# Kernel tuning notes

Hardware: AMD Instinct MI355X
Metric: run time of the kernel (lower is better)

Reference implementation:

```python
import jax, jax.numpy as jnp
import numpy as np

N_NODES, NUM_GRAPHS, MAX_N = 65536, 512, 192
D, H = 512, 8
DH = D // H


def setup_inputs() -> dict:
    key = jax.random.key(0)
    ks = jax.random.split(key, 13)
    s = 1.0 / np.sqrt(D).astype(np.float32)
    return {
        "node_features": jax.random.normal(ks[0], (N_NODES, D), jnp.float32),
        "batch_indices": jnp.sort(jax.random.randint(ks[1], (N_NODES,), 0, NUM_GRAPHS)),
        "global_query": jax.random.normal(ks[2], (1, H, 1, DH), jnp.float32) * s,
        "w_q": jax.random.normal(ks[3], (D, D), jnp.float32) * s,
        "b_q": jax.random.normal(ks[4], (D,), jnp.float32) * 0.02,
        "w_k": jax.random.normal(ks[5], (D, D), jnp.float32) * s,
        "b_k": jax.random.normal(ks[6], (D,), jnp.float32) * 0.02,
        "w_v": jax.random.normal(ks[7], (D, D), jnp.float32) * s,
        "b_v": jax.random.normal(ks[8], (D,), jnp.float32) * 0.02,
        "w_o": jax.random.normal(ks[9], (D, D), jnp.float32) * s,
        "b_o": jax.random.normal(ks[10], (D,), jnp.float32) * 0.02,
        "w_p": jax.random.normal(ks[11], (D, D), jnp.float32) * s,
        "b_p": jax.random.normal(ks[12], (D,), jnp.float32) * 0.02,
    }


def reference(node_features, batch_indices, global_query, w_q, b_q, w_k, b_k,
              w_v, b_v, w_o, b_o, w_p, b_p):
    # ragged bookkeeping (batch_indices is sorted)
    counts = jax.ops.segment_sum(jnp.ones_like(batch_indices), batch_indices,
                                 num_segments=NUM_GRAPHS)            # [G]
    offsets = jnp.cumsum(counts) - counts                            # [G]
    pos = jnp.arange(N_NODES) - offsets[batch_indices]               # local node pos

    # pad nodes to dense [G, MAX_N, D]
    dense = jnp.zeros((NUM_GRAPHS, MAX_N, D), node_features.dtype)
    dense = dense.at[batch_indices, pos].set(node_features)
    mask = jnp.zeros((NUM_GRAPHS, MAX_N), bool).at[batch_indices, pos].set(True)

    # Faithful replication of torch's expand+reshape of global_query:
    # Q_in[g, t, d] = gq_flat[h*DH + d%DH] with h = (t*D + d) // (n_g*DH)
    gqf = global_query.reshape(H * DH)
    t = jnp.arange(MAX_N)[:, None]                                   # [MAX_N,1]
    d = jnp.arange(D)[None, :]                                       # [1,D]
    n = jnp.maximum(counts, 1)[:, None, None]                        # [G,1,1]
    h = jnp.clip((t * D + d)[None] // (n * DH), 0, H - 1)            # [G,MAX_N,D]
    q_in = gqf[h * DH + (d % DH)[None]]                              # [G,MAX_N,D]

    Q = (q_in @ w_q.T + b_q).reshape(NUM_GRAPHS, MAX_N, H, DH)
    K = (dense @ w_k.T + b_k).reshape(NUM_GRAPHS, MAX_N, H, DH)
    V = (dense @ w_v.T + b_v).reshape(NUM_GRAPHS, MAX_N, H, DH)

    scale = 1.0 / np.sqrt(DH).astype(np.float32)
    scores = jnp.einsum('gthd,gshd->ghts', Q, K) * scale             # [G,H,T,S]
    scores = jnp.where(mask[:, None, None, :], scores, -1e9)
    attn_w = jax.nn.softmax(scores, axis=-1)
    attn = jnp.einsum('ghts,gshd->gthd', attn_w, V).reshape(NUM_GRAPHS, MAX_N, D)
    attn = attn @ w_o.T + b_o

    denom = jnp.maximum(counts, 1).astype(attn.dtype)[:, None]
    pooled = (attn * mask[..., None].astype(attn.dtype)).sum(axis=1) / denom
    return jax.nn.relu(pooled @ w_p.T + b_p)                         # [G, D]
```

## Files before the change

kernel.cpp:

```cpp
#include <hip/hip_runtime.h>
#include <hip/hip_bf16.h>
#include <cstdint>

typedef __bf16 bf16;
typedef __attribute__((ext_vector_type(8))) __bf16 bf16x8;
typedef __attribute__((ext_vector_type(4))) __bf16 bf16x4;
typedef __attribute__((ext_vector_type(4))) float f32x4;

#define N_NODES    65536
#define NUM_GRAPHS 512
#define MAX_N      192
#define D          512
#define H          8
#define DH         64
#define UMAX       64
#define USTRIDE    132
#define QSTRIDE    80
#define KV_LD      1024

__device__ __forceinline__ void gload_lds16(const void* g, void* l) {
    __builtin_amdgcn_global_load_lds((const __attribute__((address_space(1))) void*)g,
                                     (__attribute__((address_space(3))) void*)l, 16, 0, 0);
}

__global__ __launch_bounds__(256) void lb_kernel(const int* __restrict__ batch,
                                                 int* __restrict__ lb) {
    int g = blockIdx.x * 256 + threadIdx.x;
    if (g > NUM_GRAPHS) return;
    int lo = 0, hi = N_NODES;
    while (lo < hi) {
        int mid = (lo + hi) >> 1;
        if (batch[mid] < g) lo = mid + 1; else hi = mid;
    }
    lb[g] = lo;
}

__global__ __launch_bounds__(192) void dedup_kernel(const int* __restrict__ lb,
                                                    int* __restrict__ udata) {
    const int g = blockIdx.x;
    const int off = lb[g];
    const int n = min(lb[g + 1] - off, MAX_N);
    __shared__ int keys[MAX_N];
    const int t = threadIdx.x;
    if (t < n) {
        unsigned un = (unsigned)n;
        int key = 0;
        #pragma unroll
        for (int p = 0; p < 8; p++) key |= (int)(((unsigned)(8 * t + p)) / un) << (3 * p);
        keys[t] = key;
    }
    __syncthreads();
    if (t == 0) {
        int* base = udata + (size_t)g * USTRIDE;
        int nu = 0;
        for (int s = 0; s < n; s++) {
            if (s == 0 || keys[s] != keys[s - 1]) {
                if (nu < UMAX) { base[1 + nu] = keys[s]; base[65 + nu] = 0; nu++; }
            }
            base[65 + (nu - 1)] += 1;
        }
        base[0] = nu;
    }
}

__global__ __launch_bounds__(256) void cvt_kernel(const float* __restrict__ src,
                                                  bf16* __restrict__ dst, int n) {
    int i = (blockIdx.x * 256 + threadIdx.x) * 4;
    if (i >= n) return;
    float4 v = *(const float4*)(src + i);
    bf16x4 o = {(bf16)v.x, (bf16)v.y, (bf16)v.z, (bf16)v.w};
    *(bf16x4*)(dst + i) = o;
}

__global__ __launch_bounds__(256) void stack_bias(const float* __restrict__ bk,
                                                  const float* __restrict__ bv,
                                                  float* __restrict__ bkv) {
    int i = blockIdx.x * 256 + threadIdx.x;
    if (i < 512) bkv[i] = bk[i];
    else if (i < 1024) bkv[i] = bv[i - 512];
}

__global__ __launch_bounds__(256) void p2_kernel(const float* __restrict__ gq,
                                                 const float* __restrict__ wq,
                                                 float* __restrict__ P2) {
    int h = blockIdx.x, p = blockIdx.y;
    __shared__ float gs[64];
    if (threadIdx.x < 64) gs[threadIdx.x] = gq[h * 64 + threadIdx.x];
    __syncthreads();
    for (int o = threadIdx.x; o < D; o += 256) {
        const float* wr = wq + (size_t)o * D + p * 64;
        float acc = 0.f;
        #pragma unroll 16
        for (int j = 0; j < 64; j++) acc += gs[j] * wr[j];
        P2[(size_t)(h * 8 + p) * D + o] = acc;
    }
}

__global__ __launch_bounds__(256) void kv_gemm(const float* __restrict__ A,
                                               const bf16* __restrict__ Wkv,
                                               const float* __restrict__ bkv,
                                               bf16* __restrict__ KV) {
    const int o0 = blockIdx.x * 128;
    const int i0 = blockIdx.y * 128;
    __shared__ bf16 As[128 * 32];
    __shared__ bf16 Bs[128 * 32];
    const int tid = threadIdx.x;
    const int lane = tid & 63;
    const int w = tid >> 6;
    const int wm = w & 1, wn = w >> 1;
    const int fr = lane & 15, quad = lane >> 4;
    const int ar = tid >> 1;
    const int ac = (tid & 1) * 16;
    const float* ap0 = A + (size_t)(i0 + ar) * D + ac;
    const bf16* bp0 = Wkv + (size_t)(o0 + w * 32 + (lane >> 2)) * D + (lane & 3) * 8;

    f32x4 acc[4][4] = {};

    for (int kt = 0; kt < D; kt += 32) {
        __syncthreads();
        gload_lds16(bp0 + kt, Bs + (w * 32) * 32);
        gload_lds16(bp0 + (size_t)16 * D + kt, Bs + (w * 32 + 16) * 32);
        {
            const float* ap = ap0 + kt;
            float4 x0 = *(const float4*)ap;
            float4 x1 = *(const float4*)(ap + 4);
            float4 x2 = *(const float4*)(ap + 8);
            float4 x3 = *(const float4*)(ap + 12);
            bf16x8 v0 = {(bf16)x0.x,(bf16)x0.y,(bf16)x0.z,(bf16)x0.w,
                         (bf16)x1.x,(bf16)x1.y,(bf16)x1.z,(bf16)x1.w};
            bf16x8 v1 = {(bf16)x2.x,(bf16)x2.y,(bf16)x2.z,(bf16)x2.w,
                         (bf16)x3.x,(bf16)x3.y,(bf16)x3.z,(bf16)x3.w};
            *(bf16x8*)(As + ar * 32 + ac) = v0;
            *(bf16x8*)(As + ar * 32 + ac + 8) = v1;
        }
        __syncthreads();
        bf16x8 fa[4], fb[4];
        #pragma unroll
        for (int mf = 0; mf < 4; mf++)
            fa[mf] = *(const bf16x8*)(As + (wm * 64 + mf * 16 + fr) * 32 + quad * 8);
        #pragma unroll
        for (int nf = 0; nf < 4; nf++)
            fb[nf] = *(const bf16x8*)(Bs + (wn * 64 + nf * 16 + fr) * 32 + quad * 8);
        #pragma unroll
        for (int mf = 0; mf < 4; mf++)
            #pragma unroll
            for (int nf = 0; nf < 4; nf++)
                acc[mf][nf] = __builtin_amdgcn_mfma_f32_16x16x32_bf16(fa[mf], fb[nf], acc[mf][nf], 0, 0, 0);
    }
    #pragma unroll
    for (int nf = 0; nf < 4; nf++) {
        const int col = o0 + wn * 64 + nf * 16 + fr;
        const float bs = bkv[col];
        #pragma unroll
        for (int mf = 0; mf < 4; mf++) {
            const int row = i0 + wm * 64 + mf * 16 + quad * 4;
            #pragma unroll
            for (int r = 0; r < 4; r++)
                KV[(size_t)(row + r) * KV_LD + col] = (bf16)(acc[mf][nf][r] + bs);
        }
    }
}

__global__ __launch_bounds__(256) void attn_kernel(const bf16* __restrict__ KV,
                                                   const float* __restrict__ P2,
                                                   const float* __restrict__ bq,
                                                   const int* __restrict__ lb,
                                                   const int* __restrict__ udata,
                                                   float* __restrict__ pooled) {
    const int g = blockIdx.y;
    const int tid = threadIdx.x;
    const int lane = tid & 63;
    const int w = tid >> 6;
    const int h = blockIdx.x * 4 + w;
    const int off = lb[g];
    const int n = min(lb[g + 1] - off, MAX_N);

    __shared__ bf16 Qs[4][16 * QSTRIDE];
    __shared__ float wbar[4][MAX_N];
    __shared__ int upat_l[UMAX], ucnt_l[UMAX];

    const int* ubase = udata + (size_t)g * USTRIDE;
    const int nu = ubase[0];
    if (tid < 64) {
        upat_l[tid] = (tid < nu) ? ubase[1 + tid] : 0;
        ucnt_l[tid] = (tid < nu) ? ubase[65 + tid] : 0;
    }
    wbar[w][lane] = 0.f; wbar[w][64 + lane] = 0.f; wbar[w][128 + lane] = 0.f;
    __syncthreads();

    if (n == 0) { pooled[(size_t)g * D + h * 64 + lane] = 0.f; return; }

    const int fr = lane & 15;
    const int quad = lane >> 4;
    const float inv_n = 1.0f / (float)n;

    for (int c0 = 0; c0 < nu; c0 += 16) {
        {
            const int ul = lane >> 2;
            const int j0 = (lane & 3) * 16;
            const bool valid = (c0 + ul) < nu;
            const int pat = upat_l[c0 + ul];
            const float* bp = bq + h * 64 + j0;
            float4 q0 = *(const float4*)bp;
            float4 q1 = *(const float4*)(bp + 4);
            float4 q2 = *(const float4*)(bp + 8);
            float4 q3 = *(const float4*)(bp + 12);
            #pragma unroll
            for (int p = 0; p < 8; p++) {
                const int hp = (pat >> (3 * p)) & 7;
                const float* pp = P2 + (size_t)(hp * 8 + p) * D + h * 64 + j0;
                float4 t0 = *(const float4*)pp;
                float4 t1 = *(const float4*)(pp + 4);
                float4 t2 = *(const float4*)(pp + 8);
                float4 t3 = *(const float4*)(pp + 12);
                q0.x += t0.x; q0.y += t0.y; q0.z += t0.z; q0.w += t0.w;
                q1.x += t1.x; q1.y += t1.y; q1.z += t1.z; q1.w += t1.w;
                q2.x += t2.x; q2.y += t2.y; q2.z += t2.z; q2.w += t2.w;
                q3.x += t3.x; q3.y += t3.y; q3.z += t3.z; q3.w += t3.w;
            }
            if (!valid) {
                q0.x=q0.y=q0.z=q0.w=0.f; q1.x=q1.y=q1.z=q1.w=0.f;
                q2.x=q2.y=q2.z=q2.w=0.f; q3.x=q3.y=q3.z=q3.w=0.f;
            }
            bf16x8 b0 = {(bf16)q0.x,(bf16)q0.y,(bf16)q0.z,(bf16)q0.w,
                         (bf16)q1.x,(bf16)q1.y,(bf16)q1.z,(bf16)q1.w};
            bf16x8 b1 = {(bf16)q2.x,(bf16)q2.y,(bf16)q2.z,(bf16)q2.w,
                         (bf16)q3.x,(bf16)q3.y,(bf16)q3.z,(bf16)q3.w};
            *(bf16x8*)(&Qs[w][ul * QSTRIDE + j0])     = b0;
            *(bf16x8*)(&Qs[w][ul * QSTRIDE + j0 + 8]) = b1;
        }
        bf16x8 fa0 = *(const bf16x8*)(&Qs[w][fr * QSTRIDE + quad * 8]);
        bf16x8 fa1 = *(const bf16x8*)(&Qs[w][fr * QSTRIDE + 32 + quad * 8]);

        f32x4 sc[12];
        #pragma unroll
        for (int st = 0; st < 12; st++) {
            if (st * 16 < n) {
                int s = st * 16 + fr;
                int row = off + (s < n ? s : n - 1);
                const bf16* kp = KV + (size_t)row * KV_LD + h * 64 + quad * 8;
                bf16x8 fb0 = *(const bf16x8*)kp;
                bf16x8 fb1 = *(const bf16x8*)(kp + 32);
                f32x4 a = {0.f, 0.f, 0.f, 0.f};
                a = __builtin_amdgcn_mfma_f32_16x16x32_bf16(fa0, fb0, a, 0, 0, 0);
                a = __builtin_amdgcn_mfma_f32_16x16x32_bf16(fa1, fb1, a, 0, 0, 0);
                if (s < n) {
                    sc[st].x = a.x * 0.125f; sc[st].y = a.y * 0.125f;
                    sc[st].z = a.z * 0.125f; sc[st].w = a.w * 0.125f;
                } else {
                    sc[st].x = sc[st].y = sc[st].z = sc[st].w = -1e30f;
                }
            } else {
                sc[st].x = sc[st].y = sc[st].z = sc[st].w = -1e30f;
            }
        }
        float m[4] = {-1e30f, -1e30f, -1e30f, -1e30f};
        #pragma unroll
        for (int st = 0; st < 12; st++) {
            m[0] = fmaxf(m[0], sc[st].x); m[1] = fmaxf(m[1], sc[st].y);
            m[2] = fmaxf(m[2], sc[st].z); m[3] = fmaxf(m[3], sc[st].w);
        }
        #pragma unroll
        for (int o = 1; o <= 8; o <<= 1) {
            #pragma unroll
            for (int r = 0; r < 4; r++) m[r] = fmaxf(m[r], __shfl_xor(m[r], o));
        }
        float den[4] = {0.f, 0.f, 0.f, 0.f};
        #pragma unroll
        for (int st = 0; st < 12; st++) {
            float e0 = __expf(sc[st].x - m[0]); float e1 = __expf(sc[st].y - m[1]);
            float e2 = __expf(sc[st].z - m[2]); float e3 = __expf(sc[st].w - m[3]);
            sc[st].x = e0; sc[st].y = e1; sc[st].z = e2; sc[st].w = e3;
            den[0] += e0; den[1] += e1; den[2] += e2; den[3] += e3;
        }
        #pragma unroll
        for (int o = 1; o <= 8; o <<= 1) {
            #pragma unroll
            for (int r = 0; r < 4; r++) den[r] += __shfl_xor(den[r], o);
        }
        float wf[4];
        #pragma unroll
        for (int r = 0; r < 4; r++)
            wf[r] = (float)ucnt_l[c0 + quad * 4 + r] * inv_n / den[r];
        #pragma unroll
        for (int st = 0; st < 12; st++) {
            float v = sc[st].x * wf[0] + sc[st].y * wf[1] + sc[st].z * wf[2] + sc[st].w * wf[3];
            v += __shfl_xor(v, 16);
            v += __shfl_xor(v, 32);
            if (lane < 16) wbar[w][st * 16 + lane] += v;
        }
    }

    {
        const int jv = (lane & 15) * 4;
        const int sb = lane >> 4;
        float4 va = {0.f, 0.f, 0.f, 0.f};
        const bf16* vb = KV + 512 + h * 64 + jv;
        for (int s = sb; s < n; s += 4) {
            float wv = wbar[w][s];
            bf16x4 v4 = *(const bf16x4*)(vb + (size_t)(off + s) * KV_LD);
            va.x += wv * (float)v4[0]; va.y += wv * (float)v4[1];
            va.z += wv * (float)v4[2]; va.w += wv * (float)v4[3];
        }
        va.x += __shfl_xor(va.x, 16); va.y += __shfl_xor(va.y, 16);
        va.z += __shfl_xor(va.z, 16); va.w += __shfl_xor(va.w, 16);
        va.x += __shfl_xor(va.x, 32); va.y += __shfl_xor(va.y, 32);
        va.z += __shfl_xor(va.z, 32); va.w += __shfl_xor(va.w, 32);
        if (lane < 16) *(float4*)(pooled + (size_t)g * D + h * 64 + jv) = va;
    }
}

__global__ __launch_bounds__(256) void proj_gemm(const float* __restrict__ A,
                                                 const bf16* __restrict__ Wb,
                                                 const float* __restrict__ bias,
                                                 const int* __restrict__ lb,
                                                 int mode,
                                                 float* __restrict__ Y) {
    const int o0 = blockIdx.x * 128;
    const int i0 = blockIdx.y * 128;
    __shared__ bf16 As[128 * 32];
    __shared__ bf16 Bs[128 * 32];
    const int tid = threadIdx.x;
    const int lane = tid & 63;
    const int w = tid >> 6;
    const int wm = w & 1, wn = w >> 1;
    const int fr = lane & 15, quad = lane >> 4;
    const int ar = tid >> 1;
    const int ac = (tid & 1) * 16;
    const float* ap0 = A + (size_t)(i0 + ar) * D + ac;
    const bf16* bp0 = Wb + (size_t)(o0 + w * 32 + (lane >> 2)) * D + (lane & 3) * 8;

    f32x4 acc[4][4] = {};

    for (int kt = 0; kt < D; kt += 32) {
        __syncthreads();
        gload_lds16(bp0 + kt, Bs + (w * 32) * 32);
        gload_lds16(bp0 + (size_t)16 * D + kt, Bs + (w * 32 + 16) * 32);
        {
            const float* ap = ap0 + kt;
            float4 x0 = *(const float4*)ap;
            float4 x1 = *(const float4*)(ap + 4);
            float4 x2 = *(const float4*)(ap + 8);
            float4 x3 = *(const float4*)(ap + 12);
            bf16x8 v0 = {(bf16)x0.x,(bf16)x0.y,(bf16)x0.z,(bf16)x0.w,
                         (bf16)x1.x,(bf16)x1.y,(bf16)x1.z,(bf16)x1.w};
            bf16x8 v1 = {(bf16)x2.x,(bf16)x2.y,(bf16)x2.z,(bf16)x2.w,
                         (bf16)x3.x,(bf16)x3.y,(bf16)x3.z,(bf16)x3.w};
            *(bf16x8*)(As + ar * 32 + ac) = v0;
            *(bf16x8*)(As + ar * 32 + ac + 8) = v1;
        }
        __syncthreads();
        bf16x8 fa[4], fb[4];
        #pragma unroll
        for (int mf = 0; mf < 4; mf++)
            fa[mf] = *(const bf16x8*)(As + (wm * 64 + mf * 16 + fr) * 32 + quad * 8);
        #pragma unroll
        for (int nf = 0; nf < 4; nf++)
            fb[nf] = *(const bf16x8*)(Bs + (wn * 64 + nf * 16 + fr) * 32 + quad * 8);
        #pragma unroll
        for (int mf = 0; mf < 4; mf++)
            #pragma unroll
            for (int nf = 0; nf < 4; nf++)
                acc[mf][nf] = __builtin_amdgcn_mfma_f32_16x16x32_bf16(fa[mf], fb[nf], acc[mf][nf], 0, 0, 0);
    }
    #pragma unroll
    for (int nf = 0; nf < 4; nf++) {
        const int col = o0 + wn * 64 + nf * 16 + fr;
        const float bs = bias[col];
        #pragma unroll
        for (int mf = 0; mf < 4; mf++) {
            const int row = i0 + wm * 64 + mf * 16 + quad * 4;
            #pragma unroll
            for (int r = 0; r < 4; r++) {
                float val = acc[mf][nf][r] + bs;
                if (mode == 0) {
                    int gg = row + r;
                    if (lb[gg + 1] - lb[gg] <= 0) val = 0.f;
                } else {
                    val = fmaxf(val, 0.f);
                }
                Y[(size_t)(row + r) * D + col] = val;
            }
        }
    }
}

extern "C" void kernel_launch(void* const* d_in, const int* in_sizes, int n_in,
                              void* d_out, int out_size, void* d_ws, size_t ws_size,
                              hipStream_t stream) {
    const float* nf    = (const float*)d_in[0];
    const int*   batch = (const int*)d_in[1];
    const float* gq    = (const float*)d_in[2];
    const float* wq    = (const float*)d_in[3];
    const float* bq    = (const float*)d_in[4];
    const float* wk    = (const float*)d_in[5];
    const float* bk    = (const float*)d_in[6];
    const float* wv    = (const float*)d_in[7];
    const float* bv    = (const float*)d_in[8];
    const float* wo    = (const float*)d_in[9];
    const float* bo    = (const float*)d_in[10];
    const float* wp    = (const float*)d_in[11];
    const float* bp    = (const float*)d_in[12];
    float* out = (float*)d_out;

    char* ws = (char*)d_ws;
    bf16* KV = (bf16*)ws;
    char* p = ws + (size_t)N_NODES * KV_LD * 2;
    int*  lb   = (int*)p;      p += 4096;
    bf16* Wkvb = (bf16*)p;     p += (size_t)1024 * D * 2;
    float* bkv = (float*)p;    p += 4096;
    bf16* Wob  = (bf16*)p;     p += (size_t)D * D * 2;
    bf16* Wpb  = (bf16*)p;     p += (size_t)D * D * 2;
    float* P2  = (float*)p;    p += (size_t)64 * D * 4;
    float* pooled = (float*)p; p += (size_t)NUM_GRAPHS * D * 4;
    float* tmp = (float*)p;    p += (size_t)NUM_GRAPHS * D * 4;
    int* udata = (int*)tmp;

    lb_kernel<<<3, 256, 0, stream>>>(batch, lb);
    dedup_kernel<<<NUM_GRAPHS, 192, 0, stream>>>(lb, udata);
    cvt_kernel<<<(D * D / 4) / 256, 256, 0, stream>>>(wk, Wkvb, D * D);
    cvt_kernel<<<(D * D / 4) / 256, 256, 0, stream>>>(wv, Wkvb + (size_t)512 * D, D * D);
    cvt_kernel<<<(D * D / 4) / 256, 256, 0, stream>>>(wo, Wob, D * D);
    cvt_kernel<<<(D * D / 4) / 256, 256, 0, stream>>>(wp, Wpb, D * D);
    stack_bias<<<4, 256, 0, stream>>>(bk, bv, bkv);
    p2_kernel<<<dim3(8, 8), 256, 0, stream>>>(gq, wq, P2);
    kv_gemm<<<dim3(8, N_NODES / 128), 256, 0, stream>>>(nf, Wkvb, bkv, KV);
    attn_kernel<<<dim3(2, NUM_GRAPHS), 256, 0, stream>>>(KV, P2, bq, lb, udata, pooled);
    proj_gemm<<<dim3(4, 4), 256, 0, stream>>>(pooled, Wob, bo, lb, 0, tmp);
    proj_gemm<<<dim3(4, 4), 256, 0, stream>>>(tmp, Wpb, bp, lb, 1, out);
}
```

Baseline: 498.0 us.

## Fold V and output projections into a pooled-feature GEMM and drop V computation

Instead of computing V for every node, attention now writes per-head pooling weights. A new kernel forms per-graph, per-head weighted sums of the fp32 node features. These are multiplied by a precomputed fused Wo·Wv matrix in a split-K GEMM with atomic accumulation, and Wo·bv+bo is folded into a constant. This halves the large per-node projection GEMM and removes the V write and read. In exchange, node features are converted to bf16 in a separate full pass and read again in fp32 for the pooling, and Wo·Wv is rounded to bf16.

```diff
diff --git a/kernel.cpp b/kernel.cpp
--- a/kernel.cpp
+++ b/kernel.cpp
@@ -5,6 +5,7 @@
 typedef __bf16 bf16;
 typedef __attribute__((ext_vector_type(8))) __bf16 bf16x8;
 typedef __attribute__((ext_vector_type(4))) __bf16 bf16x4;
+typedef __attribute__((ext_vector_type(2))) __bf16 bf16x2;
 typedef __attribute__((ext_vector_type(4))) float f32x4;
 
 #define N_NODES    65536
@@ -15,8 +16,6 @@
 #define DH         64
 #define UMAX       64
 #define USTRIDE    132
-#define QSTRIDE    80
-#define KV_LD      1024
 
 __device__ __forceinline__ void gload_lds16(const void* g, void* l) {
     __builtin_amdgcn_global_load_lds((const __attribute__((address_space(1))) void*)g,
@@ -70,14 +69,6 @@
     float4 v = *(const float4*)(src + i);
     bf16x4 o = {(bf16)v.x, (bf16)v.y, (bf16)v.z, (bf16)v.w};
     *(bf16x4*)(dst + i) = o;
-}
-
-__global__ __launch_bounds__(256) void stack_bias(const float* __restrict__ bk,
-                                                  const float* __restrict__ bv,
-                                                  float* __restrict__ bkv) {
-    int i = blockIdx.x * 256 + threadIdx.x;
-    if (i < 512) bkv[i] = bk[i];
-    else if (i < 1024) bkv[i] = bv[i - 512];
 }
 
 __global__ __launch_bounds__(256) void p2_kernel(const float* __restrict__ gq,
@@ -96,12 +87,56 @@
     }
 }
 
-__global__ __launch_bounds__(256) void kv_gemm(const float* __restrict__ A,
-                                               const bf16* __restrict__ Wkv,
-                                               const float* __restrict__ bkv,
-                                               bf16* __restrict__ KV) {
-    const int o0 = blockIdx.x * 128;
-    const int i0 = blockIdx.y * 128;
+__global__ __launch_bounds__(256) void wov_kernel(const float* __restrict__ wo,
+                                                  const float* __restrict__ wv,
+                                                  bf16* __restrict__ Wov) {
+    const int ot = blockIdx.x;
+    const int h  = blockIdx.y;
+    __shared__ float wos[32 * 64];
+    for (int idx = threadIdx.x; idx < 32 * 64; idx += 256) {
+        int ol = idx >> 6, j = idx & 63;
+        wos[idx] = wo[(size_t)(ot * 32 + ol) * D + h * 64 + j];
+    }
+    __syncthreads();
+    const int c = threadIdx.x * 2;
+    float acc0[32] = {}, acc1[32] = {};
+    for (int j = 0; j < 64; j++) {
+        float2 v2 = *(const float2*)(wv + (size_t)(h * 64 + j) * D + c);
+        #pragma unroll
+        for (int o = 0; o < 32; o++) {
+            float wj = wos[o * 64 + j];
+            acc0[o] += wj * v2.x; acc1[o] += wj * v2.y;
+        }
+    }
+    #pragma unroll
+    for (int o = 0; o < 32; o++) {
+        bf16x2 r = {(bf16)acc0[o], (bf16)acc1[o]};
+        *(bf16x2*)(Wov + (size_t)(ot * 32 + o) * 4096 + h * 512 + c) = r;
+    }
+}
+
+__global__ __launch_bounds__(256) void cst_kernel(const float* __restrict__ wo,
+                                                  const float* __restrict__ bv,
+                                                  const float* __restrict__ bo,
+                                                  float* __restrict__ cst) {
+    int o = blockIdx.x * 256 + threadIdx.x;
+    if (o >= D) return;
+    const float* wr = wo + (size_t)o * D;
+    float acc = bo[o];
+    for (int d0 = 0; d0 < D; d0 += 4) {
+        float4 wv4 = *(const float4*)(wr + d0);
+        float4 b4  = *(const float4*)(bv + d0);
+        acc += wv4.x * b4.x + wv4.y * b4.y + wv4.z * b4.z + wv4.w * b4.w;
+    }
+    cst[o] = acc;
+}
+
+__global__ __launch_bounds__(256) void k_gemm(const bf16* __restrict__ Ab,
+                                              const bf16* __restrict__ Wkb,
+                                              const float* __restrict__ bkb,
+                                              bf16* __restrict__ Kout) {
+    const int i0 = blockIdx.x * 128;
+    const int o0 = blockIdx.y * 128;
     __shared__ bf16 As[128 * 32];
     __shared__ bf16 Bs[128 * 32];
     const int tid = threadIdx.x;
@@ -109,30 +144,19 @@
     const int w = tid >> 6;
     const int wm = w & 1, wn = w >> 1;
     const int fr = lane & 15, quad = lane >> 4;
-    const int ar = tid >> 1;
-    const int ac = (tid & 1) * 16;
-    const float* ap0 = A + (size_t)(i0 + ar) * D + ac;
-    const bf16* bp0 = Wkv + (size_t)(o0 + w * 32 + (lane >> 2)) * D + (lane & 3) * 8;
+    const bf16* gA = Ab + (size_t)(i0 + w * 32 + (lane >> 2)) * D + (lane & 3) * 8;
+    const bf16* gB = Wkb + (size_t)(o0 + w * 32 + (lane >> 2)) * D + (lane & 3) * 8;
+    bf16* lA = As + (w * 32) * 32;
+    bf16* lB = Bs + (w * 32) * 32;
 
     f32x4 acc[4][4] = {};
 
     for (int kt = 0; kt < D; kt += 32) {
         __syncthreads();
-        gload_lds16(bp0 + kt, Bs + (w * 32) * 32);
-        gload_lds16(bp0 + (size_t)16 * D + kt, Bs + (w * 32 + 16) * 32);
-        {
-            const float* ap = ap0 + kt;
-            float4 x0 = *(const float4*)ap;
-            float4 x1 = *(const float4*)(ap + 4);
-            float4 x2 = *(const float4*)(ap + 8);
-            float4 x3 = *(const float4*)(ap + 12);
-            bf16x8 v0 = {(bf16)x0.x,(bf16)x0.y,(bf16)x0.z,(bf16)x0.w,
-                         (bf16)x1.x,(bf16)x1.y,(bf16)x1.z,(bf16)x1.w};
-            bf16x8 v1 = {(bf16)x2.x,(bf16)x2.y,(bf16)x2.z,(bf16)x2.w,
-                         (bf16)x3.x,(bf16)x3.y,(bf16)x3.z,(bf16)x3.w};
-            *(bf16x8*)(As + ar * 32 + ac) = v0;
-            *(bf16x8*)(As + ar * 32 + ac + 8) = v1;
-        }
+        gload_lds16(gA + kt, lA);
+        gload_lds16(gA + (size_t)16 * D + kt, lA + 16 * 32);
+        gload_lds16(gB + kt, lB);
+        gload_lds16(gB + (size_t)16 * D + kt, lB + 16 * 32);
         __syncthreads();
         bf16x8 fa[4], fb[4];
         #pragma unroll
@@ -150,23 +174,23 @@
     #pragma unroll
     for (int nf = 0; nf < 4; nf++) {
         const int col = o0 + wn * 64 + nf * 16 + fr;
-        const float bs = bkv[col];
+        const float bs = bkb[col];
         #pragma unroll
         for (int mf = 0; mf < 4; mf++) {
             const int row = i0 + wm * 64 + mf * 16 + quad * 4;
             #pragma unroll
             for (int r = 0; r < 4; r++)
-                KV[(size_t)(row + r) * KV_LD + col] = (bf16)(acc[mf][nf][r] + bs);
-        }
-    }
-}
-
-__global__ __launch_bounds__(256) void attn_kernel(const bf16* __restrict__ KV,
+                Kout[(size_t)(row + r) * D + col] = (bf16)(acc[mf][nf][r] + bs);
+        }
+    }
+}
+
+__global__ __launch_bounds__(256) void attn_kernel(const bf16* __restrict__ Kb,
                                                    const float* __restrict__ P2,
                                                    const float* __restrict__ bq,
                                                    const int* __restrict__ lb,
                                                    const int* __restrict__ udata,
-                                                   float* __restrict__ pooled) {
+                                                   float* __restrict__ Wbar) {
     const int g = blockIdx.y;
     const int tid = threadIdx.x;
     const int lane = tid & 63;
@@ -175,8 +199,8 @@
     const int off = lb[g];
     const int n = min(lb[g + 1] - off, MAX_N);
 
-    __shared__ bf16 Qs[4][16 * QSTRIDE];
-    __shared__ float wbar[4][MAX_N];
+    __shared__ bf16 Qs[4][16 * 80];
+    __shared__ float wacc[4][MAX_N];
     __shared__ int upat_l[UMAX], ucnt_l[UMAX];
 
     const int* ubase = udata + (size_t)g * USTRIDE;
@@ -185,10 +209,10 @@
         upat_l[tid] = (tid < nu) ? ubase[1 + tid] : 0;
         ucnt_l[tid] = (tid < nu) ? ubase[65 + tid] : 0;
     }
-    wbar[w][lane] = 0.f; wbar[w][64 + lane] = 0.f; wbar[w][128 + lane] = 0.f;
+    wacc[w][lane] = 0.f; wacc[w][64 + lane] = 0.f; wacc[w][128 + lane] = 0.f;
     __syncthreads();
 
-    if (n == 0) { pooled[(size_t)g * D + h * 64 + lane] = 0.f; return; }
+    if (n == 0) return;
 
     const int fr = lane & 15;
     const int quad = lane >> 4;
@@ -200,11 +224,11 @@
             const int j0 = (lane & 3) * 16;
             const bool valid = (c0 + ul) < nu;
             const int pat = upat_l[c0 + ul];
-            const float* bp = bq + h * 64 + j0;
-            float4 q0 = *(const float4*)bp;
-            float4 q1 = *(const float4*)(bp + 4);
-            float4 q2 = *(const float4*)(bp + 8);
-            float4 q3 = *(const float4*)(bp + 12);
+            const float* bpq = bq + h * 64 + j0;
+            float4 q0 = *(const float4*)bpq;
+            float4 q1 = *(const float4*)(bpq + 4);
+            float4 q2 = *(const float4*)(bpq + 8);
+            float4 q3 = *(const float4*)(bpq + 12);
             #pragma unroll
             for (int p = 0; p < 8; p++) {
                 const int hp = (pat >> (3 * p)) & 7;
@@ -226,11 +250,11 @@
                          (bf16)q1.x,(bf16)q1.y,(bf16)q1.z,(bf16)q1.w};
             bf16x8 b1 = {(bf16)q2.x,(bf16)q2.y,(bf16)q2.z,(bf16)q2.w,
                          (bf16)q3.x,(bf16)q3.y,(bf16)q3.z,(bf16)q3.w};
-            *(bf16x8*)(&Qs[w][ul * QSTRIDE + j0])     = b0;
-            *(bf16x8*)(&Qs[w][ul * QSTRIDE + j0 + 8]) = b1;
-        }
-        bf16x8 fa0 = *(const bf16x8*)(&Qs[w][fr * QSTRIDE + quad * 8]);
-        bf16x8 fa1 = *(const bf16x8*)(&Qs[w][fr * QSTRIDE + 32 + quad * 8]);
+            *(bf16x8*)(&Qs[w][ul * 80 + j0])     = b0;
+            *(bf16x8*)(&Qs[w][ul * 80 + j0 + 8]) = b1;
+        }
+        bf16x8 fa0 = *(const bf16x8*)(&Qs[w][fr * 80 + quad * 8]);
+        bf16x8 fa1 = *(const bf16x8*)(&Qs[w][fr * 80 + 32 + quad * 8]);
 
         f32x4 sc[12];
         #pragma unroll
@@ -238,7 +262,7 @@
             if (st * 16 < n) {
                 int s = st * 16 + fr;
                 int row = off + (s < n ? s : n - 1);
-                const bf16* kp = KV + (size_t)row * KV_LD + h * 64 + quad * 8;
+                const bf16* kp = Kb + (size_t)row * D + h * 64 + quad * 8;
                 bf16x8 fb0 = *(const bf16x8*)kp;
                 bf16x8 fb1 = *(const bf16x8*)(kp + 32);
                 f32x4 a = {0.f, 0.f, 0.f, 0.f};
@@ -287,35 +311,115 @@
             float v = sc[st].x * wf[0] + sc[st].y * wf[1] + sc[st].z * wf[2] + sc[st].w * wf[3];
             v += __shfl_xor(v, 16);
             v += __shfl_xor(v, 32);
-            if (lane < 16) wbar[w][st * 16 + lane] += v;
-        }
-    }
-
-    {
-        const int jv = (lane & 15) * 4;
-        const int sb = lane >> 4;
-        float4 va = {0.f, 0.f, 0.f, 0.f};
-        const bf16* vb = KV + 512 + h * 64 + jv;
-        for (int s = sb; s < n; s += 4) {
-            float wv = wbar[w][s];
-            bf16x4 v4 = *(const bf16x4*)(vb + (size_t)(off + s) * KV_LD);
-            va.x += wv * (float)v4[0]; va.y += wv * (float)v4[1];
-            va.z += wv * (float)v4[2]; va.w += wv * (float)v4[3];
-        }
-        va.x += __shfl_xor(va.x, 16); va.y += __shfl_xor(va.y, 16);
-        va.z += __shfl_xor(va.z, 16); va.w += __shfl_xor(va.w, 16);
-        va.x += __shfl_xor(va.x, 32); va.y += __shfl_xor(va.y, 32);
-        va.z += __shfl_xor(va.z, 32); va.w += __shfl_xor(va.w, 32);
-        if (lane < 16) *(float4*)(pooled + (size_t)g * D + h * 64 + jv) = va;
-    }
-}
-
-__global__ __launch_bounds__(256) void proj_gemm(const float* __restrict__ A,
-                                                 const bf16* __restrict__ Wb,
-                                                 const float* __restrict__ bias,
-                                                 const int* __restrict__ lb,
-                                                 int mode,
-                                                 float* __restrict__ Y) {
+            if (lane < 16) wacc[w][st * 16 + lane] += v;
+        }
+    }
+    for (int s = lane; s < n; s += 64)
+        Wbar[(size_t)h * N_NODES + off + s] = wacc[w][s];
+}
+
+__global__ __launch_bounds__(256) void abar_kernel(const float* __restrict__ A,
+                                                   const float* __restrict__ Wbar,
+                                                   const int* __restrict__ lb,
+                                                   bf16* __restrict__ abar) {
+    const int g = blockIdx.x;
+    const int off = lb[g];
+    const int n = min(lb[g + 1] - off, MAX_N);
+    const int tid = threadIdx.x;
+    bf16* outg = abar + (size_t)g * 4096;
+    if (n == 0) {
+        bf16x2 z = {(bf16)0.f, (bf16)0.f};
+        for (int idx = tid; idx < 2048; idx += 256) *(bf16x2*)(outg + idx * 2) = z;
+        return;
+    }
+    __shared__ float wsh[MAX_N * 8];
+    for (int idx = tid; idx < n * 8; idx += 256) {
+        int s = idx >> 3, h = idx & 7;
+        wsh[idx] = Wbar[(size_t)h * N_NODES + off + s];
+    }
+    __syncthreads();
+    const int c = tid * 2;
+    float acc0[8] = {}, acc1[8] = {};
+    for (int s = 0; s < n; s++) {
+        float2 a2 = *(const float2*)(A + (size_t)(off + s) * D + c);
+        const float* wp_ = wsh + s * 8;
+        #pragma unroll
+        for (int h = 0; h < 8; h++) {
+            acc0[h] += wp_[h] * a2.x;
+            acc1[h] += wp_[h] * a2.y;
+        }
+    }
+    #pragma unroll
+    for (int h = 0; h < 8; h++) {
+        bf16x2 r = {(bf16)acc0[h], (bf16)acc1[h]};
+        *(bf16x2*)(outg + h * 512 + c) = r;
+    }
+}
+
+__global__ __launch_bounds__(256) void zero_kernel(float* __restrict__ p, int n4) {
+    int i = blockIdx.x * 256 + threadIdx.x;
+    if (i < n4) { float4 z = {0.f, 0.f, 0.f, 0.f}; *(float4*)(p + i * 4) = z; }
+}
+
+__global__ __launch_bounds__(256) void og_gemm(const bf16* __restrict__ Ab,
+                                               const bf16* __restrict__ Bb,
+                                               float* __restrict__ Yt) {
+    const int o0 = blockIdx.x * 128;
+    const int i0 = blockIdx.y * 128;
+    const int k0 = blockIdx.z * 512;
+    __shared__ bf16 As[128 * 32];
+    __shared__ bf16 Bs[128 * 32];
+    const int tid = threadIdx.x;
+    const int lane = tid & 63;
+    const int w = tid >> 6;
+    const int wm = w & 1, wn = w >> 1;
+    const int fr = lane & 15, quad = lane >> 4;
+    const bf16* gA = Ab + (size_t)(i0 + w * 32 + (lane >> 2)) * 4096 + k0 + (lane & 3) * 8;
+    const bf16* gB = Bb + (size_t)(o0 + w * 32 + (lane >> 2)) * 4096 + k0 + (lane & 3) * 8;
+    bf16* lA = As + (w * 32) * 32;
+    bf16* lB = Bs + (w * 32) * 32;
+
+    f32x4 acc[4][4] = {};
+
+    for (int kt = 0; kt < 512; kt += 32) {
+        __syncthreads();
+        gload_lds16(gA + kt, lA);
+        gload_lds16(gA + (size_t)16 * 4096 + kt, lA + 16 * 32);
+        gload_lds16(gB + kt, lB);
+        gload_lds16(gB + (size_t)16 * 4096 + kt, lB + 16 * 32);
+        __syncthreads();
+        bf16x8 fa[4], fb[4];
+        #pragma unroll
+        for (int mf = 0; mf < 4; mf++)
+            fa[mf] = *(const bf16x8*)(As + (wm * 64 + mf * 16 + fr) * 32 + quad * 8);
+        #pragma unroll
+        for (int nf = 0; nf < 4; nf++)
+            fb[nf] = *(const bf16x8*)(Bs + (wn * 64 + nf * 16 + fr) * 32 + quad * 8);
+        #pragma unroll
+        for (int mf = 0; mf < 4; mf++)
+            #pragma unroll
+            for (int nf = 0; nf < 4; nf++)
+                acc[mf][nf] = __builtin_amdgcn_mfma_f32_16x16x32_bf16(fa[mf], fb[nf], acc[mf][nf], 0, 0, 0);
+    }
+    #pragma unroll
+    for (int nf = 0; nf < 4; nf++) {
+        const int col = o0 + wn * 64 + nf * 16 + fr;
+        #pragma unroll
+        for (int mf = 0; mf < 4; mf++) {
+            const int row = i0 + wm * 64 + mf * 16 + quad * 4;
+            #pragma unroll
+            for (int r = 0; r < 4; r++)
+                atomicAdd(&Yt[(size_t)(row + r) * D + col], acc[mf][nf][r]);
+        }
+    }
+}
+
+__global__ __launch_bounds__(256) void proj_p(const float* __restrict__ tmp,
+                                              const float* __restrict__ cst,
+                                              const bf16* __restrict__ Wpb,
+                                              const float* __restrict__ bp,
+                                              const int* __restrict__ lb,
+                                              float* __restrict__ out) {
     const int o0 = blockIdx.x * 128;
     const int i0 = blockIdx.y * 128;
     __shared__ bf16 As[128 * 32];
@@ -327,25 +431,33 @@
     const int fr = lane & 15, quad = lane >> 4;
     const int ar = tid >> 1;
     const int ac = (tid & 1) * 16;
-    const float* ap0 = A + (size_t)(i0 + ar) * D + ac;
-    const bf16* bp0 = Wb + (size_t)(o0 + w * 32 + (lane >> 2)) * D + (lane & 3) * 8;
+    const int g = i0 + ar;
+    const bool live = lb[g + 1] - lb[g] > 0;
+    const float* tp = tmp + (size_t)g * D + ac;
+    const float* cp = cst + ac;
+    const bf16* gB = Wpb + (size_t)(o0 + w * 32 + (lane >> 2)) * D + (lane & 3) * 8;
+    bf16* lB = Bs + (w * 32) * 32;
 
     f32x4 acc[4][4] = {};
 
     for (int kt = 0; kt < D; kt += 32) {
         __syncthreads();
-        gload_lds16(bp0 + kt, Bs + (w * 32) * 32);
-        gload_lds16(bp0 + (size_t)16 * D + kt, Bs + (w * 32 + 16) * 32);
+        gload_lds16(gB + kt, lB);
+        gload_lds16(gB + (size_t)16 * D + kt, lB + 16 * 32);
         {
-            const float* ap = ap0 + kt;
-            float4 x0 = *(const float4*)ap;
-            float4 x1 = *(const float4*)(ap + 4);
-            float4 x2 = *(const float4*)(ap + 8);
-            float4 x3 = *(const float4*)(ap + 12);
-            bf16x8 v0 = {(bf16)x0.x,(bf16)x0.y,(bf16)x0.z,(bf16)x0.w,
-                         (bf16)x1.x,(bf16)x1.y,(bf16)x1.z,(bf16)x1.w};
-            bf16x8 v1 = {(bf16)x2.x,(bf16)x2.y,(bf16)x2.z,(bf16)x2.w,
-                         (bf16)x3.x,(bf16)x3.y,(bf16)x3.z,(bf16)x3.w};
+            float4 x0 = *(const float4*)(tp + kt);
+            float4 x1 = *(const float4*)(tp + kt + 4);
+            float4 x2 = *(const float4*)(tp + kt + 8);
+            float4 x3 = *(const float4*)(tp + kt + 12);
+            float4 c0 = *(const float4*)(cp + kt);
+            float4 c1 = *(const float4*)(cp + kt + 4);
+            float4 c2 = *(const float4*)(cp + kt + 8);
+            float4 c3 = *(const float4*)(cp + kt + 12);
+            float s = live ? 1.f : 0.f;
+            bf16x8 v0 = {(bf16)((x0.x+c0.x)*s),(bf16)((x0.y+c0.y)*s),(bf16)((x0.z+c0.z)*s),(bf16)((x0.w+c0.w)*s),
+                         (bf16)((x1.x+c1.x)*s),(bf16)((x1.y+c1.y)*s),(bf16)((x1.z+c1.z)*s),(bf16)((x1.w+c1.w)*s)};
+            bf16x8 v1 = {(bf16)((x2.x+c2.x)*s),(bf16)((x2.y+c2.y)*s),(bf16)((x2.z+c2.z)*s),(bf16)((x2.w+c2.w)*s),
+                         (bf16)((x3.x+c3.x)*s),(bf16)((x3.y+c3.y)*s),(bf16)((x3.z+c3.z)*s),(bf16)((x3.w+c3.w)*s)};
             *(bf16x8*)(As + ar * 32 + ac) = v0;
             *(bf16x8*)(As + ar * 32 + ac + 8) = v1;
         }
@@ -366,21 +478,13 @@
     #pragma unroll
     for (int nf = 0; nf < 4; nf++) {
         const int col = o0 + wn * 64 + nf * 16 + fr;
-        const float bs = bias[col];
+        const float bs = bp[col];
         #pragma unroll
         for (int mf = 0; mf < 4; mf++) {
             const int row = i0 + wm * 64 + mf * 16 + quad * 4;
             #pragma unroll
-            for (int r = 0; r < 4; r++) {
-                float val = acc[mf][nf][r] + bs;
-                if (mode == 0) {
-                    int gg = row + r;
-                    if (lb[gg + 1] - lb[gg] <= 0) val = 0.f;
-                } else {
-                    val = fmaxf(val, 0.f);
-                }
-                Y[(size_t)(row + r) * D + col] = val;
-            }
+            for (int r = 0; r < 4; r++)
+                out[(size_t)(row + r) * D + col] = fmaxf(acc[mf][nf][r] + bs, 0.f);
         }
     }
 }
@@ -404,28 +508,32 @@
     float* out = (float*)d_out;
 
     char* ws = (char*)d_ws;
-    bf16* KV = (bf16*)ws;
-    char* p = ws + (size_t)N_NODES * KV_LD * 2;
-    int*  lb   = (int*)p;      p += 4096;
-    bf16* Wkvb = (bf16*)p;     p += (size_t)1024 * D * 2;
-    float* bkv = (float*)p;    p += 4096;
-    bf16* Wob  = (bf16*)p;     p += (size_t)D * D * 2;
-    bf16* Wpb  = (bf16*)p;     p += (size_t)D * D * 2;
-    float* P2  = (float*)p;    p += (size_t)64 * D * 4;
-    float* pooled = (float*)p; p += (size_t)NUM_GRAPHS * D * 4;
-    float* tmp = (float*)p;    p += (size_t)NUM_GRAPHS * D * 4;
-    int* udata = (int*)tmp;
+    bf16*  Abf  = (bf16*)ws;
+    float* Wbar = (float*)ws;
+    bf16*  abar = (bf16*)(ws + ((size_t)2 << 20));
+    bf16*  Wov  = (bf16*)(ws + ((size_t)6 << 20));
+    float* tmp  = (float*)(ws + ((size_t)10 << 20));
+    float* cst  = (float*)(ws + ((size_t)11 << 20));
+    bf16*  Kb   = (bf16*)(ws + ((size_t)64 << 20));
+    char* sm = ws + ((size_t)128 << 20);
+    int*  lb    = (int*)sm;    sm += 4096;
+    int*  udata = (int*)sm;    sm += (size_t)NUM_GRAPHS * USTRIDE * 4 + 2048;
+    bf16* Wkb   = (bf16*)sm;   sm += (size_t)D * D * 2;
+    bf16* Wpb   = (bf16*)sm;   sm += (size_t)D * D * 2;
+    float* P2   = (float*)sm;  sm += (size_t)64 * D * 4;
 
     lb_kernel<<<3, 256, 0, stream>>>(batch, lb);
     dedup_kernel<<<NUM_GRAPHS, 192, 0, stream>>>(lb, udata);
-    cvt_kernel<<<(D * D / 4) / 256, 256, 0, stream>>>(wk, Wkvb, D * D);
-    cvt_kernel<<<(D * D / 4) / 256, 256, 0, stream>>>(wv, Wkvb + (size_t)512 * D, D * D);
-    cvt_kernel<<<(D * D / 4) / 256, 256, 0, stream>>>(wo, Wob, D * D);
+    cvt_kernel<<<(D * D / 4) / 256, 256, 0, stream>>>(wk, Wkb, D * D);
     cvt_kernel<<<(D * D / 4) / 256, 256, 0, stream>>>(wp, Wpb, D * D);
-    stack_bias<<<4, 256, 0, stream>>>(bk, bv, bkv);
     p2_kernel<<<dim3(8, 8), 256, 0, stream>>>(gq, wq, P2);
-    kv_gemm<<<dim3(8, N_NODES / 128), 256, 0, stream>>>(nf, Wkvb, bkv, KV);
-    attn_kernel<<<dim3(2, NUM_GRAPHS), 256, 0, stream>>>(KV, P2, bq, lb, udata, pooled);
-    proj_gemm<<<dim3(4, 4), 256, 0, stream>>>(pooled, Wob, bo, lb, 0, tmp);
-    proj_gemm<<<dim3(4, 4), 256, 0, stream>>>(tmp, Wpb, bp, lb, 1, out);
-}
+    cvt_kernel<<<(N_NODES * D / 4) / 256, 256, 0, stream>>>(nf, Abf, N_NODES * D);
+    k_gemm<<<dim3(N_NODES / 128, 4), 256, 0, stream>>>(Abf, Wkb, bk, Kb);
+    wov_kernel<<<dim3(16, 8), 256, 0, stream>>>(wo, wv, Wov);
+    cst_kernel<<<2, 256, 0, stream>>>(wo, bv, bo, cst);
+    attn_kernel<<<dim3(2, NUM_GRAPHS), 256, 0, stream>>>(Kb, P2, bq, lb, udata, Wbar);
+    abar_kernel<<<NUM_GRAPHS, 256, 0, stream>>>(nf, Wbar, lb, abar);
+    zero_kernel<<<(NUM_GRAPHS * D / 4 + 255) / 256, 256, 0, stream>>>(tmp, NUM_GRAPHS * D / 4);
+    og_gemm<<<dim3(4, 4, 8), 256, 0, stream>>>(abar, Wov, tmp);
+    proj_p<<<dim3(4, 4), 256, 0, stream>>>(tmp, cst, Wpb, bp, lb, out);
+}
```

After: 446.4 us. 1.12x faster.
